# Optimization experiments

Measured on AMD Instinct MI355X. Metric: run time of the kernel, lower is better.

## Reference

```python
import math
import jax, jax.numpy as jnp
import numpy as np

D_MODEL = 2048
N_HEADS = 16


def setup_inputs() -> dict:
    key = jax.random.key(0)
    ks = jax.random.split(key, 5)
    d = D_MODEL
    x = jax.random.normal(ks[0], (256, 64, d), dtype=jnp.float32)
    # nn.Linear(d, 3d): weight [3d, d], bias [3d]
    W_qkv = jax.random.normal(ks[1], (3 * d, d), dtype=jnp.float32) * (1.0 / math.sqrt(d))
    b_qkv = jnp.zeros((3 * d,), dtype=jnp.float32)
    W_out = jax.random.normal(ks[2], (d, d), dtype=jnp.float32) * (1.0 / math.sqrt(d))
    b_out = jnp.zeros((d,), dtype=jnp.float32)
    return {"x": x, "W_qkv": W_qkv, "b_qkv": b_qkv, "W_out": W_out, "b_out": b_out}


def reference(x, W_qkv, b_qkv, W_out, b_out):
    B, S, d = x.shape
    H = N_HEADS
    hd = d // H
    qkv = jnp.einsum('bsd,ed->bse', x, W_qkv) + b_qkv  # [B,S,3d]
    q, k, v = jnp.split(qkv, 3, axis=2)
    # [B,S,H,hd] -> [B,H,S,hd]
    q = q.reshape(B, S, H, hd).transpose(0, 2, 1, 3)
    k = k.reshape(B, S, H, hd).transpose(0, 2, 1, 3)
    v = v.reshape(B, S, H, hd).transpose(0, 2, 1, 3)
    attn = jnp.einsum('bhqd,bhkd->bhqk', q, k) / math.sqrt(d)  # NOTE: scaled by sqrt(d_model)
    causal = jnp.tril(jnp.ones((S, S), dtype=bool))  # [S,S]
    attn = jnp.where(causal[None, None], attn, -jnp.inf)
    # NOTE: faithful to source, softmax over dim=-2 (query axis)
    attn = jax.nn.softmax(attn, axis=-2)
    out = jnp.einsum('bhqk,bhkd->bhqd', attn, v)  # [B,H,S,hd]
    out = out.transpose(0, 2, 1, 3).reshape(B, S, d)
    return jnp.einsum('bsd,ed->bse', out, W_out) + b_out
```

## Files before the change

### kernel.cpp

```cpp
#include <hip/hip_runtime.h>
#include <hip/hip_fp16.h>

typedef _Float16 f16x8 __attribute__((ext_vector_type(8)));
typedef _Float16 f16x2 __attribute__((ext_vector_type(2)));
typedef float f32x4 __attribute__((ext_vector_type(4)));
typedef float f32x16 __attribute__((ext_vector_type(16)));
typedef short s16x8 __attribute__((ext_vector_type(8)));

typedef __attribute__((address_space(1))) void gvoid;
typedef __attribute__((address_space(3))) void lvoid;

#define GLD_LDS16(g, l) __builtin_amdgcn_global_load_lds((gvoid*)(g), (lvoid*)(l), 16, 0, 0)

__global__ __launch_bounds__(256) void cvt_f32_f16(
    const float* __restrict__ src, _Float16* __restrict__ dst, int n8)
{
    const int i = blockIdx.x * 256 + threadIdx.x;
    if (i >= n8) return;
    const float4* s = (const float4*)src;
    const float4 a = s[2 * i], b = s[2 * i + 1];
    f16x8 o;
    o[0] = (_Float16)a.x; o[1] = (_Float16)a.y; o[2] = (_Float16)a.z; o[3] = (_Float16)a.w;
    o[4] = (_Float16)b.x; o[5] = (_Float16)b.y; o[6] = (_Float16)b.z; o[7] = (_Float16)b.w;
    *(f16x8*)(dst + (size_t)i * 8) = o;
}

template <typename OutT>
__global__ __launch_bounds__(256, 4) void gemm_bt_bias(
    const _Float16* __restrict__ A, int lda,
    const _Float16* __restrict__ B,
    const float* __restrict__ bias,
    OutT* __restrict__ C, int ldc,
    int K)
{
    __shared__ alignas(16) _Float16 sA[128 * 64];
    __shared__ alignas(16) _Float16 sB[128 * 64];

    const int t = threadIdx.x;
    const int lane = t & 63, wave = t >> 6;
    const int m0 = blockIdx.y * 128, n0 = blockIdx.x * 128;
    const int wm = wave >> 1, wn = wave & 1;
    const int l31 = lane & 31, kh = lane >> 5;

    f32x16 acc[2][2];
#pragma unroll
    for (int i = 0; i < 2; ++i)
#pragma unroll
        for (int j = 0; j < 2; ++j)
#pragma unroll
            for (int r = 0; r < 16; ++r) acc[i][j][r] = 0.f;

    const _Float16* gA[4];
    const _Float16* gB[4];
#pragma unroll
    for (int g = 0; g < 4; ++g) {
        const int s = (wave * 4 + g) * 64 + lane;
        const int r = s >> 3;
        const int c = (s & 7) ^ (r & 7);
        gA[g] = A + (size_t)(m0 + r) * lda + c * 8;
        gB[g] = B + (size_t)(n0 + r) * K + c * 8;
    }

    const int ar0 = wm * 64 + l31, ar1 = ar0 + 32;
    const int br0 = wn * 64 + l31, br1 = br0 + 32;
    const int swa = ar0 & 7, swb = br0 & 7;

    for (int k0 = 0; k0 < K; k0 += 64) {
#pragma unroll
        for (int g = 0; g < 4; ++g) {
            GLD_LDS16(gA[g], sA + (wave * 4 + g) * 512);
            GLD_LDS16(gB[g], sB + (wave * 4 + g) * 512);
            gA[g] += 64; gB[g] += 64;
        }
        __syncthreads();

#pragma unroll
        for (int s = 0; s < 4; ++s) {
            const int ck = 2 * s + kh;
            const f16x8 a0 = *(const f16x8*)(sA + ar0 * 64 + ((ck ^ swa) * 8));
            const f16x8 a1 = *(const f16x8*)(sA + ar1 * 64 + ((ck ^ swa) * 8));
            const f16x8 b0 = *(const f16x8*)(sB + br0 * 64 + ((ck ^ swb) * 8));
            const f16x8 b1 = *(const f16x8*)(sB + br1 * 64 + ((ck ^ swb) * 8));
            acc[0][0] = __builtin_amdgcn_mfma_f32_32x32x16_f16(a0, b0, acc[0][0], 0, 0, 0);
            acc[0][1] = __builtin_amdgcn_mfma_f32_32x32x16_f16(a0, b1, acc[0][1], 0, 0, 0);
            acc[1][0] = __builtin_amdgcn_mfma_f32_32x32x16_f16(a1, b0, acc[1][0], 0, 0, 0);
            acc[1][1] = __builtin_amdgcn_mfma_f32_32x32x16_f16(a1, b1, acc[1][1], 0, 0, 0);
        }
        __syncthreads();
    }

#pragma unroll
    for (int nt = 0; nt < 2; ++nt) {
        const int col = n0 + wn * 64 + nt * 32 + l31;
        const float bs = bias[col];
#pragma unroll
        for (int mt = 0; mt < 2; ++mt) {
#pragma unroll
            for (int reg = 0; reg < 16; ++reg) {
                const int row = m0 + wm * 64 + mt * 32 + 4 * kh + (reg & 3) + 8 * (reg >> 2);
                C[(size_t)row * ldc + col] = (OutT)(acc[mt][nt][reg] + bs);
            }
        }
    }
}

__global__ __launch_bounds__(256) void attn_fused(_Float16* __restrict__ qkv)
{
    constexpr float SCALE = 0.022097086912079608f;
    __shared__ alignas(16) char smem[51968];
    __shared__ float sRed[256];
    _Float16* sQ = (_Float16*)smem;
    _Float16* sK = (_Float16*)(smem + 17408);
    _Float16* sV = (_Float16*)(smem + 34816);
    float* sSt = (float*)smem;
    _Float16* sP = (_Float16*)(smem + 17408);

    const int t = threadIdx.x;
    const int bh = blockIdx.x;
    const int b = bh >> 4, h = bh & 15;
    const int ld = 6144;
    const _Float16* Qg = qkv + (size_t)b * 64 * ld + h * 128;
    const _Float16* Kg = Qg + 2048;
    const _Float16* Vg = Qg + 4096;
    _Float16* Og = qkv + (size_t)b * 64 * ld + h * 128;

    for (int i = t; i < 1024; i += 256) {
        const int r = i >> 4, c = (i & 15) * 8;
        *(s16x8*)(sQ + r * 136 + c) = *(const s16x8*)(Qg + (size_t)r * ld + c);
        *(s16x8*)(sK + r * 136 + c) = *(const s16x8*)(Kg + (size_t)r * ld + c);
        const f16x8 vv = *(const f16x8*)(Vg + (size_t)r * ld + c);
#pragma unroll
        for (int p = 0; p < 4; ++p) {
            f16x2 w2; w2[0] = vv[2 * p]; w2[1] = vv[2 * p + 1];
            *(f16x2*)(sV + r * 134 + c + 2 * p) = w2;
        }
    }
    __syncthreads();

    const int lane = t & 63, w = t >> 6;
    const int l15 = lane & 15, q4 = lane >> 4;
    const f32x4 fz = {0.f, 0.f, 0.f, 0.f};

    f32x4 sc[4];
#pragma unroll
    for (int nt = 0; nt < 4; ++nt) sc[nt] = fz;
#pragma unroll
    for (int kk = 0; kk < 128; kk += 32) {
        const f16x8 aq = *(const f16x8*)(sQ + (w * 16 + l15) * 136 + kk + q4 * 8);
#pragma unroll
        for (int nt = 0; nt < 4; ++nt) {
            const f16x8 bk = *(const f16x8*)(sK + (nt * 16 + l15) * 136 + kk + q4 * 8);
            sc[nt] = __builtin_amdgcn_mfma_f32_16x16x32_f16(aq, bk, sc[nt], 0, 0, 0);
        }
    }
    __syncthreads();

#pragma unroll
    for (int nt = 0; nt < 4; ++nt)
#pragma unroll
        for (int i = 0; i < 4; ++i)
            sSt[(nt * 16 + l15) * 65 + (w * 16 + q4 * 4 + i)] = sc[nt][i] * SCALE;
    __syncthreads();

    {
        const int k = t >> 2, j = t & 3;
        const int qlo = max(k, j * 16), qhi = min(64, j * 16 + 16);
        float mx = -3.0e38f;
        for (int q = qlo; q < qhi; ++q) mx = fmaxf(mx, sSt[k * 65 + q]);
        sRed[t] = mx;
        __syncthreads();
        mx = fmaxf(fmaxf(sRed[k * 4 + 0], sRed[k * 4 + 1]),
                   fmaxf(sRed[k * 4 + 2], sRed[k * 4 + 3]));
        float sum = 0.f;
        for (int q = qlo; q < qhi; ++q) {
            const float e = __expf(sSt[k * 65 + q] - mx);
            sSt[k * 65 + q] = e;
            sum += e;
        }
        sRed[t] = sum;
        __syncthreads();
        const float inv = 1.f / (sRed[k * 4 + 0] + sRed[k * 4 + 1] +
                                 sRed[k * 4 + 2] + sRed[k * 4 + 3]);
        for (int q = j * 16; q < j * 16 + 16; ++q) {
            const float p = (q >= k) ? sSt[k * 65 + q] * inv : 0.f;
            sP[q * 72 + k] = (_Float16)p;
        }
    }
    __syncthreads();

    f32x4 oa[8];
#pragma unroll
    for (int nt = 0; nt < 8; ++nt) oa[nt] = fz;
#pragma unroll
    for (int kk = 0; kk < 64; kk += 32) {
        const f16x8 ap = *(const f16x8*)(sP + (w * 16 + l15) * 72 + kk + q4 * 8);
#pragma unroll
        for (int nt = 0; nt < 8; ++nt) {
            f16x8 bv;
#pragma unroll
            for (int j = 0; j < 8; ++j)
                bv[j] = sV[(kk + q4 * 8 + j) * 134 + nt * 16 + l15];
            oa[nt] = __builtin_amdgcn_mfma_f32_16x16x32_f16(ap, bv, oa[nt], 0, 0, 0);
        }
    }
#pragma unroll
    for (int nt = 0; nt < 8; ++nt)
#pragma unroll
        for (int i = 0; i < 4; ++i)
            Og[(size_t)(w * 16 + q4 * 4 + i) * ld + nt * 16 + l15] =
                (_Float16)(oa[nt][i]);
}

extern "C" void kernel_launch(void* const* d_in, const int* in_sizes, int n_in,
                              void* d_out, int out_size, void* d_ws, size_t ws_size,
                              hipStream_t stream) {
    const float* x     = (const float*)d_in[0];
    const float* W_qkv = (const float*)d_in[1];
    const float* b_qkv = (const float*)d_in[2];
    const float* W_out = (const float*)d_in[3];
    const float* b_out = (const float*)d_in[4];
    float* out = (float*)d_out;

    char* ws = (char*)d_ws;
    _Float16* qkv = (_Float16*)ws;
    _Float16* xh  = (_Float16*)(ws + 201326592);
    _Float16* wqh = (_Float16*)(ws + 268435456);
    _Float16* woh = wqh;

    cvt_f32_f16<<<dim3(33554432 / 2048), 256, 0, stream>>>(x, xh, 33554432 / 8);
    cvt_f32_f16<<<dim3(12582912 / 2048), 256, 0, stream>>>(W_qkv, wqh, 12582912 / 8);
    gemm_bt_bias<_Float16><<<dim3(48, 128), 256, 0, stream>>>(
        xh, 2048, wqh, b_qkv, qkv, 6144, 2048);
    cvt_f32_f16<<<dim3(4194304 / 2048), 256, 0, stream>>>(W_out, woh, 4194304 / 8);
    attn_fused<<<dim3(4096), 256, 0, stream>>>(qkv);
    gemm_bt_bias<float><<<dim3(16, 128), 256, 0, stream>>>(
        qkv, 6144, woh, b_out, out, 2048, 2048);
}
```

Baseline: 953.9 us.

## Rewrite GEMM as 256x256 double-buffered pipelined kernel with block swizzle

Replaces the 128x128 single-buffered GEMM with a 256x256-tile, 512-thread kernel that double-buffers LDS and interleaves global-to-LDS loads for the next K tile with MFMA work on the current one. Waves are prioritized with setprio during MFMA, and the block index is remapped across groups of eight for better L2 locality. The aim is to hide memory latency and raise arithmetic intensity for both projection GEMMs. In exchange it uses 128KB LDS and a large accumulator set, so only one block fits per CU and there are fewer blocks in total.

```diff
diff --git a/kernel.cpp b/kernel.cpp
--- a/kernel.cpp
+++ b/kernel.cpp
@@ -4,13 +4,13 @@
 typedef _Float16 f16x8 __attribute__((ext_vector_type(8)));
 typedef _Float16 f16x2 __attribute__((ext_vector_type(2)));
 typedef float f32x4 __attribute__((ext_vector_type(4)));
-typedef float f32x16 __attribute__((ext_vector_type(16)));
 typedef short s16x8 __attribute__((ext_vector_type(8)));
 
 typedef __attribute__((address_space(1))) void gvoid;
 typedef __attribute__((address_space(3))) void lvoid;
 
 #define GLD_LDS16(g, l) __builtin_amdgcn_global_load_lds((gvoid*)(g), (lvoid*)(l), 16, 0, 0)
+#define BAR() __builtin_amdgcn_s_barrier()
 
 __global__ __launch_bounds__(256) void cvt_f32_f16(
     const float* __restrict__ src, _Float16* __restrict__ dst, int n8)
@@ -26,80 +26,150 @@
 }
 
 template <typename OutT>
-__global__ __launch_bounds__(256, 4) void gemm_bt_bias(
+__global__ __launch_bounds__(512, 1) void gemm_bt_bias(
     const _Float16* __restrict__ A, int lda,
     const _Float16* __restrict__ B,
     const float* __restrict__ bias,
     OutT* __restrict__ C, int ldc,
-    int K)
+    int K, int nbx)
 {
-    __shared__ alignas(16) _Float16 sA[128 * 64];
-    __shared__ alignas(16) _Float16 sB[128 * 64];
-
-    const int t = threadIdx.x;
-    const int lane = t & 63, wave = t >> 6;
-    const int m0 = blockIdx.y * 128, n0 = blockIdx.x * 128;
-    const int wm = wave >> 1, wn = wave & 1;
-    const int l31 = lane & 31, kh = lane >> 5;
-
-    f32x16 acc[2][2];
-#pragma unroll
-    for (int i = 0; i < 2; ++i)
-#pragma unroll
-        for (int j = 0; j < 2; ++j)
-#pragma unroll
-            for (int r = 0; r < 16; ++r) acc[i][j][r] = 0.f;
-
-    const _Float16* gA[4];
-    const _Float16* gB[4];
-#pragma unroll
-    for (int g = 0; g < 4; ++g) {
-        const int s = (wave * 4 + g) * 64 + lane;
-        const int r = s >> 3;
-        const int c = (s & 7) ^ (r & 7);
-        gA[g] = A + (size_t)(m0 + r) * lda + c * 8;
-        gB[g] = B + (size_t)(n0 + r) * K + c * 8;
-    }
-
-    const int ar0 = wm * 64 + l31, ar1 = ar0 + 32;
-    const int br0 = wn * 64 + l31, br1 = br0 + 32;
-    const int swa = ar0 & 7, swb = br0 & 7;
-
-    for (int k0 = 0; k0 < K; k0 += 64) {
-#pragma unroll
-        for (int g = 0; g < 4; ++g) {
-            GLD_LDS16(gA[g], sA + (wave * 4 + g) * 512);
-            GLD_LDS16(gB[g], sB + (wave * 4 + g) * 512);
-            gA[g] += 64; gB[g] += 64;
-        }
-        __syncthreads();
-
-#pragma unroll
-        for (int s = 0; s < 4; ++s) {
-            const int ck = 2 * s + kh;
-            const f16x8 a0 = *(const f16x8*)(sA + ar0 * 64 + ((ck ^ swa) * 8));
-            const f16x8 a1 = *(const f16x8*)(sA + ar1 * 64 + ((ck ^ swa) * 8));
-            const f16x8 b0 = *(const f16x8*)(sB + br0 * 64 + ((ck ^ swb) * 8));
-            const f16x8 b1 = *(const f16x8*)(sB + br1 * 64 + ((ck ^ swb) * 8));
-            acc[0][0] = __builtin_amdgcn_mfma_f32_32x32x16_f16(a0, b0, acc[0][0], 0, 0, 0);
-            acc[0][1] = __builtin_amdgcn_mfma_f32_32x32x16_f16(a0, b1, acc[0][1], 0, 0, 0);
-            acc[1][0] = __builtin_amdgcn_mfma_f32_32x32x16_f16(a1, b0, acc[1][0], 0, 0, 0);
-            acc[1][1] = __builtin_amdgcn_mfma_f32_32x32x16_f16(a1, b1, acc[1][1], 0, 0, 0);
-        }
-        __syncthreads();
-    }
-
-#pragma unroll
-    for (int nt = 0; nt < 2; ++nt) {
-        const int col = n0 + wn * 64 + nt * 32 + l31;
+    __shared__ alignas(16) _Float16 smem[65536];
+
+    const int tid = threadIdx.x;
+    const int lane = tid & 63, wv = tid >> 6;
+    const int nwg = gridDim.x;
+    int bid = blockIdx.x;
+    if ((nwg & 7) == 0) bid = (bid & 7) * (nwg >> 3) + (bid >> 3);
+    const int m0 = (bid / nbx) * 256, n0 = (bid % nbx) * 256;
+    const int wm = wv >> 2, wn = wv & 3;
+    const int l15 = lane & 15, q4 = lane >> 4, l7 = lane & 7;
+    const int nk = K >> 6;
+
+    const int rl = tid >> 3;
+    const int cl = (tid & 7) ^ (rl & 7);
+    const _Float16* gp00 = A + (size_t)(m0 + rl) * lda + cl * 8;
+    const _Float16* gp01 = A + (size_t)(m0 + 64 + rl) * lda + cl * 8;
+    const _Float16* gp10 = A + (size_t)(m0 + 128 + rl) * lda + cl * 8;
+    const _Float16* gp11 = A + (size_t)(m0 + 192 + rl) * lda + cl * 8;
+    const _Float16* gp20 = B + (size_t)(n0 + rl) * (size_t)K + cl * 8;
+    const _Float16* gp21 = B + (size_t)(n0 + 64 + rl) * (size_t)K + cl * 8;
+    const _Float16* gp30 = B + (size_t)(n0 + 128 + rl) * (size_t)K + cl * 8;
+    const _Float16* gp31 = B + (size_t)(n0 + 192 + rl) * (size_t)K + cl * 8;
+
+    f32x4 acc[8][4];
+#pragma unroll
+    for (int i = 0; i < 8; ++i)
+#pragma unroll
+        for (int j = 0; j < 4; ++j)
+            acc[i][j] = (f32x4){0.f, 0.f, 0.f, 0.f};
+
+    f16x8 fa[4][2], fb0[2][2], fb1[2][2];
+
+#define STAGE(J, tile_) do {                                                  \
+    const int dd_ = (tile_) & 1;                                              \
+    _Float16* lb_ = &smem[dd_ * 32768 + ((J) >> 1) * 16384 +                  \
+                          ((J) & 1) * 8192 + wv * 512];                       \
+    const size_t ko_ = (size_t)(tile_) * 64;                                  \
+    GLD_LDS16(gp##J##0 + ko_, lb_);                                           \
+    GLD_LDS16(gp##J##1 + ko_, lb_ + 4096);                                    \
+} while (0)
+
+#define RD_A(d_, mq_) do {                                                    \
+    const _Float16* ba_ = &smem[(d_) * 32768];                                \
+    _Pragma("unroll")                                                         \
+    for (int fi = 0; fi < 4; ++fi) {                                          \
+        const int r_ = wm * 128 + (mq_) * 64 + fi * 16 + l15;                 \
+        fa[fi][0] = *(const f16x8*)(ba_ + r_ * 64 + ((q4 ^ l7) * 8));         \
+        fa[fi][1] = *(const f16x8*)(ba_ + r_ * 64 + (((4 + q4) ^ l7) * 8));   \
+    }                                                                         \
+} while (0)
+
+#define RD_B(d_, nq_, fbv) do {                                               \
+    const _Float16* bb_ = &smem[(d_) * 32768 + 16384];                        \
+    _Pragma("unroll")                                                         \
+    for (int fj = 0; fj < 2; ++fj) {                                          \
+        const int r_ = wn * 64 + (nq_) * 32 + fj * 16 + l15;                  \
+        fbv[fj][0] = *(const f16x8*)(bb_ + r_ * 64 + ((q4 ^ l7) * 8));        \
+        fbv[fj][1] = *(const f16x8*)(bb_ + r_ * 64 + (((4 + q4) ^ l7) * 8));  \
+    }                                                                         \
+} while (0)
+
+#define MM(mq_, nq_, fbv) do {                                                \
+    __builtin_amdgcn_s_setprio(1);                                            \
+    _Pragma("unroll")                                                         \
+    for (int ks = 0; ks < 2; ++ks)                                            \
+    _Pragma("unroll")                                                         \
+    for (int fi = 0; fi < 4; ++fi)                                            \
+    _Pragma("unroll")                                                         \
+    for (int fj = 0; fj < 2; ++fj)                                            \
+        acc[(mq_) * 4 + fi][(nq_) * 2 + fj] =                                 \
+            __builtin_amdgcn_mfma_f32_16x16x32_f16(                           \
+                fa[fi][ks], fbv[fj][ks],                                      \
+                acc[(mq_) * 4 + fi][(nq_) * 2 + fj], 0, 0, 0);                \
+    __builtin_amdgcn_s_setprio(0);                                            \
+} while (0)
+
+#define GTILE(d_, S1, S2, S3, S4, VMN) do {                                   \
+    RD_A(d_, 0); RD_B(d_, 0, fb0);                                           \
+    S1;                                                                       \
+    BAR(); MM(0, 0, fb0); BAR();                                              \
+    RD_B(d_, 1, fb1);                                                         \
+    S2;                                                                       \
+    BAR(); MM(0, 1, fb1); BAR();                                              \
+    RD_A(d_, 1);                                                              \
+    S3;                                                                       \
+    BAR(); MM(1, 1, fb1); BAR();                                              \
+    S4;                                                                       \
+    BAR(); MM(1, 0, fb0);                                                     \
+    asm volatile("s_waitcnt vmcnt(" #VMN ")" ::: "memory");                   \
+    BAR();                                                                    \
+} while (0)
+
+    STAGE(0, 0); STAGE(1, 0); STAGE(2, 0); STAGE(3, 0);
+    if (nk > 1) {
+        STAGE(0, 1);
+        asm volatile("s_waitcnt vmcnt(2)" ::: "memory");
+    } else {
+        asm volatile("s_waitcnt vmcnt(0)" ::: "memory");
+    }
+    BAR();
+
+    for (int kt = 0; kt < nk - 2; ++kt) {
+        const int d = kt & 1;
+        GTILE(d, STAGE(1, kt + 1), STAGE(2, kt + 1), STAGE(3, kt + 1),
+              STAGE(0, kt + 2), 2);
+    }
+    if (nk >= 2) {
+        GTILE((nk - 2) & 1, STAGE(1, nk - 1), STAGE(2, nk - 1),
+              STAGE(3, nk - 1), (void)0, 0);
+    }
+    {
+        const int d = (nk - 1) & 1;
+        RD_A(d, 0); RD_B(d, 0, fb0);
+        MM(0, 0, fb0);
+        RD_B(d, 1, fb1);
+        MM(0, 1, fb1);
+        RD_A(d, 1);
+        MM(1, 1, fb1);
+        MM(1, 0, fb0);
+    }
+
+#undef GTILE
+#undef MM
+#undef RD_B
+#undef RD_A
+#undef STAGE
+
+#pragma unroll
+    for (int nj = 0; nj < 4; ++nj) {
+        const int col = n0 + wn * 64 + nj * 16 + l15;
         const float bs = bias[col];
 #pragma unroll
-        for (int mt = 0; mt < 2; ++mt) {
-#pragma unroll
-            for (int reg = 0; reg < 16; ++reg) {
-                const int row = m0 + wm * 64 + mt * 32 + 4 * kh + (reg & 3) + 8 * (reg >> 2);
-                C[(size_t)row * ldc + col] = (OutT)(acc[mt][nt][reg] + bs);
-            }
+        for (int mi = 0; mi < 8; ++mi) {
+            const int row = m0 + wm * 128 + mi * 16 + q4 * 4;
+#pragma unroll
+            for (int i = 0; i < 4; ++i)
+                C[(size_t)(row + i) * ldc + col] = (OutT)(acc[mi][nj][i] + bs);
         }
     }
 }
@@ -229,10 +299,10 @@
 
     cvt_f32_f16<<<dim3(33554432 / 2048), 256, 0, stream>>>(x, xh, 33554432 / 8);
     cvt_f32_f16<<<dim3(12582912 / 2048), 256, 0, stream>>>(W_qkv, wqh, 12582912 / 8);
-    gemm_bt_bias<_Float16><<<dim3(48, 128), 256, 0, stream>>>(
-        xh, 2048, wqh, b_qkv, qkv, 6144, 2048);
+    gemm_bt_bias<_Float16><<<dim3(1536), 512, 0, stream>>>(
+        xh, 2048, wqh, b_qkv, qkv, 6144, 2048, 24);
     cvt_f32_f16<<<dim3(4194304 / 2048), 256, 0, stream>>>(W_out, woh, 4194304 / 8);
     attn_fused<<<dim3(4096), 256, 0, stream>>>(qkv);
-    gemm_bt_bias<float><<<dim3(16, 128), 256, 0, stream>>>(
-        qkv, 6144, woh, b_out, out, 2048, 2048);
+    gemm_bt_bias<float><<<dim3(512), 512, 0, stream>>>(
+        qkv, 6144, woh, b_out, out, 2048, 2048, 8);
 }
```

After: 842.1 us. 1.13x faster.
